# Optimization experiments

Hardware: AMD Instinct MI355X
Metric: run time of the kernel (lower is better)

Reference implementation:

```python
import jax, jax.numpy as jnp
import numpy as np

B, T, W_DIM = 32, 2048, 1024
G, D = 16, 64          # num_groups, input_dim (w = G*D)
MOM = 0.9
TH = 0.5
EPS = 1e-8
TOP_K = 2


def setup_inputs() -> dict:
    key = jax.random.key(0)
    k = jax.random.split(key, 4)
    x = jax.random.normal(k[0], (B, T, W_DIM), dtype=jnp.float32)
    ema = jnp.zeros((W_DIM, W_DIM), dtype=jnp.float32)
    W1 = jax.random.normal(k[1], (G, 16, D), dtype=jnp.float32) * 0.05
    b1 = jnp.zeros((G, 16), dtype=jnp.float32)
    W2 = jax.random.normal(k[2], (G, 1, 16), dtype=jnp.float32) * 0.05
    b2 = jnp.zeros((G, 1), dtype=jnp.float32)
    return {"x": x, "ema": ema, "W1": W1, "b1": b1, "W2": W2, "b2": b2}


def _corr_over_T(x):
    # x: (B, T, w) -> per-batch Pearson corr over the T axis: (B, w, w)
    Tn = x.shape[1]
    c = x - x.mean(axis=1, keepdims=True)
    cov = jnp.einsum('btw,btv->bwv', c, c) / (Tn - 1)
    std = jnp.sqrt(jnp.sum(c * c, axis=1) / (Tn - 1))  # (B, w)
    return jnp.clip(cov / (std[:, :, None] * std[:, None, :] + EPS), -1.0, 1.0)


def reference(x, ema, W1, b1, W2, b2):
    # --- burst-masked EMA update (torch.no_grad) ---
    corr_batch = jax.lax.stop_gradient(_corr_over_T(x))  # (B, w, w)

    def step(e, c):
        mask = jnp.abs(c) > TH
        return jnp.where(mask, MOM * e + (1.0 - MOM) * c, e), None

    ema_new, _ = jax.lax.scan(step, ema, corr_batch)

    # --- split into groups: (B, T, G, D) ---
    Bn, Tn, w = x.shape
    groups = x.reshape(Bn, Tn, G, D)

    # --- per-group correlation score: mean |off-diagonal| of within-group corr ---
    cg = groups - groups.mean(axis=1, keepdims=True)
    cov_g = jnp.einsum('btgd,btge->bgde', cg, cg) / (Tn - 1)        # (B, G, D, D)
    std_g = jnp.sqrt(jnp.sum(cg * cg, axis=1) / (Tn - 1))           # (B, G, D)
    corr_g = jnp.clip(cov_g / (std_g[..., :, None] * std_g[..., None, :] + EPS), -1.0, 1.0)
    absc = jnp.abs(corr_g)
    offdiag = (absc.sum(axis=(-2, -1)) - jnp.einsum('bgdd->bg', absc)) / (D * D - D)
    correlations = offdiag.mean(axis=0)                              # (G,)

    # --- select the 2 least-correlated groups (these get gradients) ---
    _, sel = jax.lax.top_k(-correlations, TOP_K)
    sel_mask = jnp.zeros((G,), dtype=bool).at[sel].set(True)

    # --- per-group expert MLP: D -> 16 -> 1, batched over groups ---
    h = jax.nn.relu(jnp.einsum('btgd,ghd->btgh', groups, W1) + b1)   # (B, T, G, 16)
    o = (jnp.einsum('btgh,goh->btgo', h, W2) + b2)[..., 0]           # (B, T, G)

    # non-selected groups run under no_grad -> stop_gradient on their outputs
    out = jnp.where(sel_mask[None, None, :], o, jax.lax.stop_gradient(o))
    return out, correlations, ema_new
```

## Files before the change

### kernel.cpp

```cpp
#include <hip/hip_runtime.h>
#include <hip/hip_bf16.h>
#include <stdint.h>

#define B_   32
#define T_   2048
#define W_   1024
#define G_   16
#define D_   64
#define LIST_CAP 65536
#define BK   64

typedef __bf16 bf16_t;
typedef __bf16 bf16x8 __attribute__((ext_vector_type(8)));
typedef float  f32x4  __attribute__((ext_vector_type(4)));

#define WS_XT      0ull
#define WS_XT_SZ   (134217728ull)
#define WS_SUM     (WS_XT + WS_XT_SZ)
#define WS_SQ      (WS_SUM + 131072ull)
#define WS_MU      (WS_SQ  + 131072ull)
#define WS_SIG     (WS_MU  + 131072ull)
#define WS_ACCUM   (WS_SIG + 131072ull)
#define WS_LISTCNT (WS_ACCUM + 256ull)
#define WS_LIST    (WS_LISTCNT + 256ull)
#define WS_MASK    (WS_LIST + 1048576ull)
#define WS_DIAG    (WS_MASK + 4194304ull)

__global__ __launch_bounds__(256) void stats_transpose(
    const float* __restrict__ x, bf16_t* __restrict__ xT,
    float* __restrict__ sumb, float* __restrict__ sqb) {
  int b = blockIdx.z, t0 = blockIdx.x * 64, w0 = blockIdx.y * 64;
  __shared__ float tile[64][65];
  __shared__ float rs[64][17], rq[64][17];
  int tid = threadIdx.x;
  int wc = tid & 15, tr = tid >> 4;
  float4 s4 = {0.f, 0.f, 0.f, 0.f}, q4 = {0.f, 0.f, 0.f, 0.f};
  const float4* xp = (const float4*)(x + ((size_t)b * T_ + t0) * W_ + w0);
#pragma unroll
  for (int p = 0; p < 4; ++p) {
    int t = tr + 16 * p;
    float4 v = xp[(size_t)t * 256 + wc];
    s4.x += v.x; s4.y += v.y; s4.z += v.z; s4.w += v.w;
    q4.x += v.x * v.x; q4.y += v.y * v.y; q4.z += v.z * v.z; q4.w += v.w * v.w;
    tile[4 * wc + 0][t] = v.x;
    tile[4 * wc + 1][t] = v.y;
    tile[4 * wc + 2][t] = v.z;
    tile[4 * wc + 3][t] = v.w;
  }
  rs[4 * wc + 0][tr] = s4.x; rs[4 * wc + 1][tr] = s4.y;
  rs[4 * wc + 2][tr] = s4.z; rs[4 * wc + 3][tr] = s4.w;
  rq[4 * wc + 0][tr] = q4.x; rq[4 * wc + 1][tr] = q4.y;
  rq[4 * wc + 2][tr] = q4.z; rq[4 * wc + 3][tr] = q4.w;
  __syncthreads();
  if (tid < 64) {
    float s = 0.f, q = 0.f;
#pragma unroll
    for (int i = 0; i < 16; ++i) { s += rs[tid][i]; q += rq[tid][i]; }
    atomicAdd(&sumb[b * W_ + w0 + tid], s);
    atomicAdd(&sqb[b * W_ + w0 + tid], q);
  }
  int c = tid & 7, wv = tid >> 3;
#pragma unroll
  for (int p = 0; p < 2; ++p) {
    int w = wv + 32 * p;
    const float* src = &tile[w][c * 8];
    bf16x8 o;
#pragma unroll
    for (int k = 0; k < 8; ++k) o[k] = (bf16_t)src[k];
    *(bf16x8*)(xT + ((size_t)b * W_ + w0 + w) * T_ + t0 + c * 8) = o;
  }
}

__global__ void finalize_stats(const float* __restrict__ sumb,
                               const float* __restrict__ sqb,
                               float* __restrict__ mu, float* __restrict__ sig) {
  int idx = blockIdx.x * 256 + threadIdx.x;
  float s = sumb[idx], q = sqb[idx];
  float m = s * (1.0f / 2048.0f);
  float var = (q - s * m) * (1.0f / 2047.0f);
  if (var < 0.f) var = 0.f;
  mu[idx] = m;
  sig[idx] = sqrtf(var);
}

__global__ __launch_bounds__(256) void gram_kernel(
    const bf16_t* __restrict__ xT, const float* __restrict__ mu,
    const float* __restrict__ sig, unsigned int* __restrict__ mask,
    float* __restrict__ diagv, int* __restrict__ listcnt,
    int4* __restrict__ list, float* __restrict__ accum) {
  int id = blockIdx.x;
  int xcd = id & 7;
  int idx = id >> 3;
  int sub = idx / 36;
  int rt  = idx % 36;
  int b = sub * 8 + xcd;
  int r = rt, ti = 0;
  while (r >= 8 - ti) { r -= 8 - ti; ++ti; }
  int tj = ti + r;
  int i0 = ti * 128, j0 = tj * 128;

  const bf16_t* Ag = xT + ((size_t)b * W_ + i0) * T_;
  const bf16_t* Bg = xT + ((size_t)b * W_ + j0) * T_;

  __shared__ __attribute__((aligned(16))) bf16_t As[128 * BK];
  __shared__ __attribute__((aligned(16))) bf16_t Bs[128 * BK];

  int tid = threadIdx.x;
  int lane = tid & 63, wave = tid >> 6;
  int wm = wave >> 1, wn = wave & 1;

  f32x4 zero = {0.f, 0.f, 0.f, 0.f};
  f32x4 acc[4][4];
#pragma unroll
  for (int mi = 0; mi < 4; ++mi)
#pragma unroll
    for (int nj = 0; nj < 4; ++nj) acc[mi][nj] = zero;

  int arow = wm * 64 + (lane & 15);
  int brow = wn * 64 + (lane & 15);
  int q = lane >> 4;

  for (int k0 = 0; k0 < T_; k0 += BK) {
    __syncthreads();
#pragma unroll
    for (int s = 0; s < 4; ++s) {
      int c = s * 256 + tid;
      int row = c >> 3, slot = c & 7;
      int gslot = slot ^ (row & 7);
      __builtin_amdgcn_global_load_lds(
          (const __attribute__((address_space(1))) void*)(Ag + (size_t)row * T_ + k0 + gslot * 8),
          (__attribute__((address_space(3))) void*)(As + c * 8), 16, 0, 0);
      __builtin_amdgcn_global_load_lds(
          (const __attribute__((address_space(1))) void*)(Bg + (size_t)row * T_ + k0 + gslot * 8),
          (__attribute__((address_space(3))) void*)(Bs + c * 8), 16, 0, 0);
    }
    __syncthreads();

#pragma unroll
    for (int s2 = 0; s2 < 2; ++s2) {
      bf16x8 af[4], bfr[4];
#pragma unroll
      for (int mi = 0; mi < 4; ++mi) {
        int row = arow + mi * 16;
        af[mi] = *(const bf16x8*)(As + row * BK + ((s2 * 4 + q) ^ (row & 7)) * 8);
      }
#pragma unroll
      for (int nj = 0; nj < 4; ++nj) {
        int row = brow + nj * 16;
        bfr[nj] = *(const bf16x8*)(Bs + row * BK + ((s2 * 4 + q) ^ (row & 7)) * 8);
      }
#pragma unroll
      for (int mi = 0; mi < 4; ++mi)
#pragma unroll
        for (int nj = 0; nj < 4; ++nj)
          acc[mi][nj] = __builtin_amdgcn_mfma_f32_16x16x32_bf16(af[mi], bfr[nj], acc[mi][nj], 0, 0, 0);
    }
  }

  const float inv = 1.0f / 2047.0f;
  const float* mub = mu + b * W_;
  const float* sgb = sig + b * W_;
  bool diagquad = (ti == tj) && (wm == wn);
  float gsum = 0.f;

#pragma unroll
  for (int nj = 0; nj < 4; ++nj) {
    int j = j0 + wn * 64 + nj * 16 + (lane & 15);
    float muj = mub[j], sgj = sgb[j];
#pragma unroll
    for (int mi = 0; mi < 4; ++mi) {
#pragma unroll
      for (int rr = 0; rr < 4; ++rr) {
        int i = i0 + wm * 64 + mi * 16 + (lane >> 4) * 4 + rr;
        float cov = (acc[mi][nj][rr] - 2048.0f * mub[i] * muj) * inv;
        float corr = cov / (sgb[i] * sgj + 1e-8f);
        corr = fminf(1.0f, fmaxf(-1.0f, corr));
        if (diagquad && (i != j)) gsum += fabsf(corr);
        if (fabsf(corr) > 0.5f) {
          atomicOr(&mask[i * W_ + j], 1u << b);
          if (i == j) {
            diagv[b * W_ + i] = corr;
          } else {
            int p = atomicAdd(listcnt, 1);
            if (p < LIST_CAP) list[p] = make_int4(b, i, j, __float_as_int(corr));
          }
          if (ti != tj) {
            atomicOr(&mask[j * W_ + i], 1u << b);
            int p = atomicAdd(listcnt, 1);
            if (p < LIST_CAP) list[p] = make_int4(b, j, i, __float_as_int(corr));
          }
        }
      }
    }
  }
  if (diagquad) {
    for (int o = 32; o > 0; o >>= 1) gsum += __shfl_down(gsum, o);
    if (lane == 0) atomicAdd(&accum[ti * 2 + wm], gsum);
  }
}

__global__ void ema_kernel(const float* __restrict__ ema,
                           const unsigned int* __restrict__ mask,
                           const float* __restrict__ diagv,
                           const int* __restrict__ listcnt,
                           const int4* __restrict__ list,
                           float* __restrict__ emaout) {
  int idx = blockIdx.x * 256 + threadIdx.x;
  int i = idx >> 10, j = idx & 1023;
  float e = ema[idx];
  unsigned int m = mask[idx];
  if (m) {
    if (i == j) {
      for (int b = 0; b < 32; ++b)
        if ((m >> b) & 1u) e = 0.9f * e + 0.1f * diagv[b * W_ + i];
    } else {
      int cnt = *listcnt; if (cnt > LIST_CAP) cnt = LIST_CAP;
      for (int b = 0; b < 32; ++b) {
        if ((m >> b) & 1u) {
          for (int k = 0; k < cnt; ++k) {
            int4 t = list[k];
            if (t.x == b && t.y == i && t.z == j) {
              e = 0.9f * e + 0.1f * __int_as_float(t.w);
              break;
            }
          }
        }
      }
    }
  }
  emaout[idx] = e;
}

__global__ void corr_finalize(const float* __restrict__ accum, float* __restrict__ outc) {
  int g = threadIdx.x;
  if (g < 16) outc[g] = accum[g] * (1.0f / (32.0f * 4032.0f));
}

__global__ __launch_bounds__(256) void mlp_kernel(
    const float* __restrict__ x, const float* __restrict__ W1,
    const float* __restrict__ b1, const float* __restrict__ W2,
    const float* __restrict__ b2, float* __restrict__ out) {
  int b = blockIdx.y, t0 = blockIdx.x * 64, gs = blockIdx.z * 4;
  int tid = threadIdx.x;
  int gl = tid & 3, tl = tid >> 2;
  __shared__ float Wt[16 * 64 * 4];
  __shared__ float b1s[16 * 4], W2s[16 * 4], b2s[4];
  for (int l = tid; l < 4096; l += 256) {
    int g2 = l & 3, jd = l >> 2;
    Wt[l] = W1[(size_t)(gs + g2) * 1024 + jd];
  }
  if (tid < 64) {
    int g2 = tid & 3, j = tid >> 2;
    b1s[j * 4 + g2] = b1[(gs + g2) * 16 + j];
    W2s[j * 4 + g2] = W2[(gs + g2) * 16 + j];
  }
  if (tid < 4) b2s[tid] = b2[gs + tid];
  __syncthreads();

  int g = gs + gl, t = t0 + tl;
  const float4* xp = (const float4*)(x + ((size_t)b * T_ + t) * W_ + g * D_);
  float h[16];
#pragma unroll
  for (int j = 0; j < 16; ++j) h[j] = b1s[j * 4 + gl];
#pragma unroll
  for (int d4 = 0; d4 < 16; ++d4) {
    float4 xv = xp[d4];
#pragma unroll
    for (int j = 0; j < 16; ++j) {
      const float* wp = &Wt[(j * 64 + d4 * 4) * 4 + gl];
      h[j] += xv.x * wp[0] + xv.y * wp[4] + xv.z * wp[8] + xv.w * wp[12];
    }
  }
  float o = b2s[gl];
#pragma unroll
  for (int j = 0; j < 16; ++j) o += fmaxf(h[j], 0.f) * W2s[j * 4 + gl];
  out[((size_t)b * T_ + t) * 16 + g] = o;
}

extern "C" void kernel_launch(void* const* d_in, const int* in_sizes, int n_in,
                              void* d_out, int out_size, void* d_ws, size_t ws_size,
                              hipStream_t stream) {
  const float* x   = (const float*)d_in[0];
  const float* ema = (const float*)d_in[1];
  const float* W1  = (const float*)d_in[2];
  const float* b1  = (const float*)d_in[3];
  const float* W2  = (const float*)d_in[4];
  const float* b2  = (const float*)d_in[5];

  float* out    = (float*)d_out;
  float* outc   = out + 1048576;
  float* outema = outc + 16;

  char* ws = (char*)d_ws;
  bf16_t* xT        = (bf16_t*)(ws + WS_XT);
  float* sumb       = (float*)(ws + WS_SUM);
  float* sqb        = (float*)(ws + WS_SQ);
  float* mub        = (float*)(ws + WS_MU);
  float* sigb       = (float*)(ws + WS_SIG);
  float* accum      = (float*)(ws + WS_ACCUM);
  int*   listcnt    = (int*)(ws + WS_LISTCNT);
  int4*  list       = (int4*)(ws + WS_LIST);
  unsigned int* msk = (unsigned int*)(ws + WS_MASK);
  float* diagv      = (float*)(ws + WS_DIAG);

  hipMemsetAsync(ws + WS_SUM, 0, 262144, stream);
  hipMemsetAsync(ws + WS_ACCUM, 0, 512, stream);
  hipMemsetAsync(ws + WS_MASK, 0, 4194304, stream);

  stats_transpose<<<dim3(32, 16, 32), 256, 0, stream>>>(x, xT, sumb, sqb);
  finalize_stats<<<128, 256, 0, stream>>>(sumb, sqb, mub, sigb);
  gram_kernel<<<1152, 256, 0, stream>>>(xT, mub, sigb, msk, diagv, listcnt, list, accum);
  ema_kernel<<<4096, 256, 0, stream>>>(ema, msk, diagv, listcnt, list, outema);
  corr_finalize<<<1, 16, 0, stream>>>(accum, outc);
  mlp_kernel<<<dim3(32, 32, 4), 256, 0, stream>>>(x, W1, b1, W2, b2, out);
}
```

Before: 728.0 us.

## Fuse stats/memsets into transpose, double-buffer gram, restructure MLP, merge small kernels

Stats_transpose now loops over all T per block, computing mean and std directly. It also zeroes the mask, accum and list counter, which removes the memsets, the atomics and the finalize kernel. The gram kernel uses a double-buffered LDS pipeline with K-step 32 so loads overlap MFMA work. The corr finalize is folded into the ema kernel. The MLP kernel is restructured to load all weights once and split D across 4 lanes with shuffle reductions. Fewer blocks in the transpose may reduce memory parallelism.

```diff
diff --git a/kernel.cpp b/kernel.cpp
--- a/kernel.cpp
+++ b/kernel.cpp
@@ -5,10 +5,7 @@
 #define B_   32
 #define T_   2048
 #define W_   1024
-#define G_   16
-#define D_   64
 #define LIST_CAP 65536
-#define BK   64
 
 typedef __bf16 bf16_t;
 typedef __bf16 bf16x8 __attribute__((ext_vector_type(8)));
@@ -16,9 +13,7 @@
 
 #define WS_XT      0ull
 #define WS_XT_SZ   (134217728ull)
-#define WS_SUM     (WS_XT + WS_XT_SZ)
-#define WS_SQ      (WS_SUM + 131072ull)
-#define WS_MU      (WS_SQ  + 131072ull)
+#define WS_MU      (WS_XT + WS_XT_SZ)
 #define WS_SIG     (WS_MU  + 131072ull)
 #define WS_ACCUM   (WS_SIG + 131072ull)
 #define WS_LISTCNT (WS_ACCUM + 256ull)
@@ -28,24 +23,53 @@
 
 __global__ __launch_bounds__(256) void stats_transpose(
     const float* __restrict__ x, bf16_t* __restrict__ xT,
-    float* __restrict__ sumb, float* __restrict__ sqb) {
-  int b = blockIdx.z, t0 = blockIdx.x * 64, w0 = blockIdx.y * 64;
+    float* __restrict__ mu, float* __restrict__ sig,
+    unsigned int* __restrict__ mask, float* __restrict__ accum,
+    int* __restrict__ listcnt) {
+  int b = blockIdx.y, w0 = blockIdx.x * 64;
+  int bid = blockIdx.y * 16 + blockIdx.x;
+  int tid = threadIdx.x;
+  {
+    uint4* m4 = (uint4*)mask + (size_t)bid * 512;
+    uint4 z = {0u, 0u, 0u, 0u};
+#pragma unroll
+    for (int i = 0; i < 2; ++i) m4[tid + 256 * i] = z;
+    if (bid == 0) {
+      if (tid < 16) accum[tid] = 0.f;
+      if (tid == 16) *listcnt = 0;
+    }
+  }
   __shared__ float tile[64][65];
   __shared__ float rs[64][17], rq[64][17];
-  int tid = threadIdx.x;
   int wc = tid & 15, tr = tid >> 4;
   float4 s4 = {0.f, 0.f, 0.f, 0.f}, q4 = {0.f, 0.f, 0.f, 0.f};
-  const float4* xp = (const float4*)(x + ((size_t)b * T_ + t0) * W_ + w0);
-#pragma unroll
-  for (int p = 0; p < 4; ++p) {
-    int t = tr + 16 * p;
-    float4 v = xp[(size_t)t * 256 + wc];
-    s4.x += v.x; s4.y += v.y; s4.z += v.z; s4.w += v.w;
-    q4.x += v.x * v.x; q4.y += v.y * v.y; q4.z += v.z * v.z; q4.w += v.w * v.w;
-    tile[4 * wc + 0][t] = v.x;
-    tile[4 * wc + 1][t] = v.y;
-    tile[4 * wc + 2][t] = v.z;
-    tile[4 * wc + 3][t] = v.w;
+  const float4* xp = (const float4*)(x + (size_t)b * T_ * W_ + w0);
+  int wrc = tid & 7, wv = tid >> 3;
+
+  for (int tc = 0; tc < 32; ++tc) {
+    int t0 = tc * 64;
+    __syncthreads();
+#pragma unroll
+    for (int p = 0; p < 4; ++p) {
+      int t = tr + 16 * p;
+      float4 v = xp[(size_t)(t0 + t) * 256 + wc];
+      s4.x += v.x; s4.y += v.y; s4.z += v.z; s4.w += v.w;
+      q4.x += v.x * v.x; q4.y += v.y * v.y; q4.z += v.z * v.z; q4.w += v.w * v.w;
+      tile[4 * wc + 0][t] = v.x;
+      tile[4 * wc + 1][t] = v.y;
+      tile[4 * wc + 2][t] = v.z;
+      tile[4 * wc + 3][t] = v.w;
+    }
+    __syncthreads();
+#pragma unroll
+    for (int p = 0; p < 2; ++p) {
+      int w = wv + 32 * p;
+      const float* src = &tile[w][wrc * 8];
+      bf16x8 o;
+#pragma unroll
+      for (int k = 0; k < 8; ++k) o[k] = (bf16_t)src[k];
+      *(bf16x8*)(xT + ((size_t)b * W_ + w0 + w) * T_ + t0 + wrc * 8) = o;
+    }
   }
   rs[4 * wc + 0][tr] = s4.x; rs[4 * wc + 1][tr] = s4.y;
   rs[4 * wc + 2][tr] = s4.z; rs[4 * wc + 3][tr] = s4.w;
@@ -56,31 +80,12 @@
     float s = 0.f, q = 0.f;
 #pragma unroll
     for (int i = 0; i < 16; ++i) { s += rs[tid][i]; q += rq[tid][i]; }
-    atomicAdd(&sumb[b * W_ + w0 + tid], s);
-    atomicAdd(&sqb[b * W_ + w0 + tid], q);
-  }
-  int c = tid & 7, wv = tid >> 3;
-#pragma unroll
-  for (int p = 0; p < 2; ++p) {
-    int w = wv + 32 * p;
-    const float* src = &tile[w][c * 8];
-    bf16x8 o;
-#pragma unroll
-    for (int k = 0; k < 8; ++k) o[k] = (bf16_t)src[k];
-    *(bf16x8*)(xT + ((size_t)b * W_ + w0 + w) * T_ + t0 + c * 8) = o;
-  }
-}
-
-__global__ void finalize_stats(const float* __restrict__ sumb,
-                               const float* __restrict__ sqb,
-                               float* __restrict__ mu, float* __restrict__ sig) {
-  int idx = blockIdx.x * 256 + threadIdx.x;
-  float s = sumb[idx], q = sqb[idx];
-  float m = s * (1.0f / 2048.0f);
-  float var = (q - s * m) * (1.0f / 2047.0f);
-  if (var < 0.f) var = 0.f;
-  mu[idx] = m;
-  sig[idx] = sqrtf(var);
+    float m = s * (1.0f / 2048.0f);
+    float var = (q - s * m) * (1.0f / 2047.0f);
+    if (var < 0.f) var = 0.f;
+    mu[b * W_ + w0 + tid] = m;
+    sig[b * W_ + w0 + tid] = sqrtf(var);
+  }
 }
 
 __global__ __launch_bounds__(256) void gram_kernel(
@@ -102,8 +107,8 @@
   const bf16_t* Ag = xT + ((size_t)b * W_ + i0) * T_;
   const bf16_t* Bg = xT + ((size_t)b * W_ + j0) * T_;
 
-  __shared__ __attribute__((aligned(16))) bf16_t As[128 * BK];
-  __shared__ __attribute__((aligned(16))) bf16_t Bs[128 * BK];
+  __shared__ __attribute__((aligned(16))) bf16_t As[2][128 * 32];
+  __shared__ __attribute__((aligned(16))) bf16_t Bs[2][128 * 32];
 
   int tid = threadIdx.x;
   int lane = tid & 63, wave = tid >> 6;
@@ -120,42 +125,50 @@
   int brow = wn * 64 + (lane & 15);
   int q = lane >> 4;
 
-  for (int k0 = 0; k0 < T_; k0 += BK) {
+  int c0 = tid, c1 = 256 + tid;
+  int row0 = c0 >> 2, sl0 = (c0 & 3) ^ (row0 & 3) ^ ((row0 >> 2) & 3);
+  int row1 = c1 >> 2, sl1 = (c1 & 3) ^ (row1 & 3) ^ ((row1 >> 2) & 3);
+
+#define STAGE(p, k0)                                                                   \
+  do {                                                                                 \
+    __builtin_amdgcn_global_load_lds(                                                  \
+        (const __attribute__((address_space(1))) void*)(Ag + (size_t)row0 * T_ + (k0) + sl0 * 8), \
+        (__attribute__((address_space(3))) void*)(&As[p][c0 * 8]), 16, 0, 0);          \
+    __builtin_amdgcn_global_load_lds(                                                  \
+        (const __attribute__((address_space(1))) void*)(Bg + (size_t)row0 * T_ + (k0) + sl0 * 8), \
+        (__attribute__((address_space(3))) void*)(&Bs[p][c0 * 8]), 16, 0, 0);          \
+    __builtin_amdgcn_global_load_lds(                                                  \
+        (const __attribute__((address_space(1))) void*)(Ag + (size_t)row1 * T_ + (k0) + sl1 * 8), \
+        (__attribute__((address_space(3))) void*)(&As[p][c1 * 8]), 16, 0, 0);          \
+    __builtin_amdgcn_global_load_lds(                                                  \
+        (const __attribute__((address_space(1))) void*)(Bg + (size_t)row1 * T_ + (k0) + sl1 * 8), \
+        (__attribute__((address_space(3))) void*)(&Bs[p][c1 * 8]), 16, 0, 0);          \
+  } while (0)
+
+  STAGE(0, 0);
+#pragma unroll 2
+  for (int it = 0; it < 64; ++it) {
+    int p = it & 1;
     __syncthreads();
-#pragma unroll
-    for (int s = 0; s < 4; ++s) {
-      int c = s * 256 + tid;
-      int row = c >> 3, slot = c & 7;
-      int gslot = slot ^ (row & 7);
-      __builtin_amdgcn_global_load_lds(
-          (const __attribute__((address_space(1))) void*)(Ag + (size_t)row * T_ + k0 + gslot * 8),
-          (__attribute__((address_space(3))) void*)(As + c * 8), 16, 0, 0);
-      __builtin_amdgcn_global_load_lds(
-          (const __attribute__((address_space(1))) void*)(Bg + (size_t)row * T_ + k0 + gslot * 8),
-          (__attribute__((address_space(3))) void*)(Bs + c * 8), 16, 0, 0);
-    }
-    __syncthreads();
-
-#pragma unroll
-    for (int s2 = 0; s2 < 2; ++s2) {
-      bf16x8 af[4], bfr[4];
-#pragma unroll
-      for (int mi = 0; mi < 4; ++mi) {
-        int row = arow + mi * 16;
-        af[mi] = *(const bf16x8*)(As + row * BK + ((s2 * 4 + q) ^ (row & 7)) * 8);
-      }
-#pragma unroll
-      for (int nj = 0; nj < 4; ++nj) {
-        int row = brow + nj * 16;
-        bfr[nj] = *(const bf16x8*)(Bs + row * BK + ((s2 * 4 + q) ^ (row & 7)) * 8);
-      }
-#pragma unroll
-      for (int mi = 0; mi < 4; ++mi)
-#pragma unroll
-        for (int nj = 0; nj < 4; ++nj)
-          acc[mi][nj] = __builtin_amdgcn_mfma_f32_16x16x32_bf16(af[mi], bfr[nj], acc[mi][nj], 0, 0, 0);
-    }
-  }
+    if (it < 63) STAGE(p ^ 1, (it + 1) * 32);
+    bf16x8 af[4], bfr[4];
+#pragma unroll
+    for (int mi = 0; mi < 4; ++mi) {
+      int row = arow + mi * 16;
+      af[mi] = *(const bf16x8*)(&As[p][row * 32 + ((q ^ (row & 3) ^ ((row >> 2) & 3)) * 8)]);
+    }
+#pragma unroll
+    for (int nj = 0; nj < 4; ++nj) {
+      int row = brow + nj * 16;
+      bfr[nj] = *(const bf16x8*)(&Bs[p][row * 32 + ((q ^ (row & 3) ^ ((row >> 2) & 3)) * 8)]);
+    }
+#pragma unroll
+    for (int mi = 0; mi < 4; ++mi)
+#pragma unroll
+      for (int nj = 0; nj < 4; ++nj)
+        acc[mi][nj] = __builtin_amdgcn_mfma_f32_16x16x32_bf16(af[mi], bfr[nj], acc[mi][nj], 0, 0, 0);
+  }
+#undef STAGE
 
   const float inv = 1.0f / 2047.0f;
   const float* mub = mu + b * W_;
@@ -181,13 +194,13 @@
           if (i == j) {
             diagv[b * W_ + i] = corr;
           } else {
-            int p = atomicAdd(listcnt, 1);
-            if (p < LIST_CAP) list[p] = make_int4(b, i, j, __float_as_int(corr));
+            int p2 = atomicAdd(listcnt, 1);
+            if (p2 < LIST_CAP) list[p2] = make_int4(b, i, j, __float_as_int(corr));
           }
           if (ti != tj) {
             atomicOr(&mask[j * W_ + i], 1u << b);
-            int p = atomicAdd(listcnt, 1);
-            if (p < LIST_CAP) list[p] = make_int4(b, j, i, __float_as_int(corr));
+            int p2 = atomicAdd(listcnt, 1);
+            if (p2 < LIST_CAP) list[p2] = make_int4(b, j, i, __float_as_int(corr));
           }
         }
       }
@@ -204,7 +217,11 @@
                            const float* __restrict__ diagv,
                            const int* __restrict__ listcnt,
                            const int4* __restrict__ list,
-                           float* __restrict__ emaout) {
+                           float* __restrict__ emaout,
+                           const float* __restrict__ accum,
+                           float* __restrict__ outc) {
+  if (blockIdx.x == 0 && threadIdx.x < 16)
+    outc[threadIdx.x] = accum[threadIdx.x] * (1.0f / (32.0f * 4032.0f));
   int idx = blockIdx.x * 256 + threadIdx.x;
   int i = idx >> 10, j = idx & 1023;
   float e = ema[idx];
@@ -231,50 +248,71 @@
   emaout[idx] = e;
 }
 
-__global__ void corr_finalize(const float* __restrict__ accum, float* __restrict__ outc) {
-  int g = threadIdx.x;
-  if (g < 16) outc[g] = accum[g] * (1.0f / (32.0f * 4032.0f));
-}
-
-__global__ __launch_bounds__(256) void mlp_kernel(
+__global__ void mlp_kernel(
     const float* __restrict__ x, const float* __restrict__ W1,
     const float* __restrict__ b1, const float* __restrict__ W2,
     const float* __restrict__ b2, float* __restrict__ out) {
-  int b = blockIdx.y, t0 = blockIdx.x * 64, gs = blockIdx.z * 4;
+  __shared__ float4 W1s4[4112];
+  __shared__ float b1s[256], W2s[256], b2s[16];
   int tid = threadIdx.x;
-  int gl = tid & 3, tl = tid >> 2;
-  __shared__ float Wt[16 * 64 * 4];
-  __shared__ float b1s[16 * 4], W2s[16 * 4], b2s[4];
-  for (int l = tid; l < 4096; l += 256) {
-    int g2 = l & 3, jd = l >> 2;
-    Wt[l] = W1[(size_t)(gs + g2) * 1024 + jd];
-  }
-  if (tid < 64) {
-    int g2 = tid & 3, j = tid >> 2;
-    b1s[j * 4 + g2] = b1[(gs + g2) * 16 + j];
-    W2s[j * 4 + g2] = W2[(gs + g2) * 16 + j];
-  }
-  if (tid < 4) b2s[tid] = b2[gs + tid];
+  const float4* W1f4 = (const float4*)W1;
+#pragma unroll
+  for (int p = 0; p < 16; ++p) {
+    int idx = tid + 256 * p;
+    W1s4[idx + (idx >> 8)] = W1f4[idx];
+  }
+  b1s[tid] = b1[tid];
+  W2s[tid] = W2[tid];
+  if (tid < 16) b2s[tid] = b2[tid];
   __syncthreads();
 
-  int g = gs + gl, t = t0 + tl;
-  const float4* xp = (const float4*)(x + ((size_t)b * T_ + t) * W_ + g * D_);
-  float h[16];
-#pragma unroll
-  for (int j = 0; j < 16; ++j) h[j] = b1s[j * 4 + gl];
-#pragma unroll
-  for (int d4 = 0; d4 < 16; ++d4) {
-    float4 xv = xp[d4];
+  int dl = tid & 3, g = (tid >> 2) & 15, tp = tid >> 6;
+  size_t bt0 = (size_t)blockIdx.x * 16 + tp * 4;
+  const float4* xf4 = (const float4*)x;
+
+  float4 xv[4][4];
+#pragma unroll
+  for (int i = 0; i < 4; ++i)
+#pragma unroll
+    for (int c = 0; c < 4; ++c)
+      xv[i][c] = xf4[(bt0 + i) * 256 + g * 16 + dl * 4 + c];
+
+  float ph[4][16];
+#pragma unroll
+  for (int i = 0; i < 4; ++i)
+#pragma unroll
+    for (int j = 0; j < 16; ++j) ph[i][j] = 0.f;
+
+  const float4* wbase = &W1s4[g * 257 + dl * 4];
+#pragma unroll
+  for (int j = 0; j < 16; ++j) {
+    float4 w0 = wbase[j * 16 + 0];
+    float4 w1 = wbase[j * 16 + 1];
+    float4 w2 = wbase[j * 16 + 2];
+    float4 w3 = wbase[j * 16 + 3];
+#pragma unroll
+    for (int i = 0; i < 4; ++i) {
+      float a = xv[i][0].x * w0.x + xv[i][0].y * w0.y + xv[i][0].z * w0.z + xv[i][0].w * w0.w;
+      a += xv[i][1].x * w1.x + xv[i][1].y * w1.y + xv[i][1].z * w1.z + xv[i][1].w * w1.w;
+      a += xv[i][2].x * w2.x + xv[i][2].y * w2.y + xv[i][2].z * w2.z + xv[i][2].w * w2.w;
+      a += xv[i][3].x * w3.x + xv[i][3].y * w3.y + xv[i][3].z * w3.z + xv[i][3].w * w3.w;
+      ph[i][j] += a;
+    }
+  }
+
+#pragma unroll
+  for (int i = 0; i < 4; ++i) {
+    float o = b2s[g];
 #pragma unroll
     for (int j = 0; j < 16; ++j) {
-      const float* wp = &Wt[(j * 64 + d4 * 4) * 4 + gl];
-      h[j] += xv.x * wp[0] + xv.y * wp[4] + xv.z * wp[8] + xv.w * wp[12];
-    }
-  }
-  float o = b2s[gl];
-#pragma unroll
-  for (int j = 0; j < 16; ++j) o += fmaxf(h[j], 0.f) * W2s[j * 4 + gl];
-  out[((size_t)b * T_ + t) * 16 + g] = o;
+      float v = ph[i][j];
+      v += __shfl_xor(v, 1);
+      v += __shfl_xor(v, 2);
+      v += b1s[g * 16 + j];
+      o += fmaxf(v, 0.f) * W2s[g * 16 + j];
+    }
+    if (dl == 0) out[(bt0 + i) * 16 + g] = o;
+  }
 }
 
 extern "C" void kernel_launch(void* const* d_in, const int* in_sizes, int n_in,
@@ -293,8 +331,6 @@
 
   char* ws = (char*)d_ws;
   bf16_t* xT        = (bf16_t*)(ws + WS_XT);
-  float* sumb       = (float*)(ws + WS_SUM);
-  float* sqb        = (float*)(ws + WS_SQ);
   float* mub        = (float*)(ws + WS_MU);
   float* sigb       = (float*)(ws + WS_SIG);
   float* accum      = (float*)(ws + WS_ACCUM);
@@ -303,14 +339,8 @@
   unsigned int* msk = (unsigned int*)(ws + WS_MASK);
   float* diagv      = (float*)(ws + WS_DIAG);
 
-  hipMemsetAsync(ws + WS_SUM, 0, 262144, stream);
-  hipMemsetAsync(ws + WS_ACCUM, 0, 512, stream);
-  hipMemsetAsync(ws + WS_MASK, 0, 4194304, stream);
-
-  stats_transpose<<<dim3(32, 16, 32), 256, 0, stream>>>(x, xT, sumb, sqb);
-  finalize_stats<<<128, 256, 0, stream>>>(sumb, sqb, mub, sigb);
+  stats_transpose<<<dim3(16, 32), 256, 0, stream>>>(x, xT, mub, sigb, msk, accum, listcnt);
   gram_kernel<<<1152, 256, 0, stream>>>(xT, mub, sigb, msk, diagv, listcnt, list, accum);
-  ema_kernel<<<4096, 256, 0, stream>>>(ema, msk, diagv, listcnt, list, outema);
-  corr_finalize<<<1, 16, 0, stream>>>(accum, outc);
-  mlp_kernel<<<dim3(32, 32, 4), 256, 0, stream>>>(x, W1, b1, W2, b2, out);
-}
+  ema_kernel<<<4096, 256, 0, stream>>>(ema, msk, diagv, listcnt, list, outema, accum, outc);
+  mlp_kernel<<<4096, 256, 0, stream>>>(x, W1, b1, W2, b2, out);
+}
```

Measured after the change: 1.362 ms. +87.0%, slower.
